# Kernel tuning notes

Hardware: AMD Instinct MI355X
Metric: run time of the kernel (lower is better)

Reference implementation:

```python
import jax, jax.numpy as jnp
import numpy as np

S, B, H, DIN = 2048, 64, 1024, 1024

def setup_inputs() -> dict:
    key = jax.random.key(0)
    ks = jax.random.split(key, 6)
    return {
        "x": jax.random.normal(ks[0], (1, B, DIN), dtype=jnp.float32),
        "last_hidden": jax.random.normal(ks[1], (1, B, H), dtype=jnp.float32),
        "encoder_outputs": jax.random.normal(ks[2], (S, B, H), dtype=jnp.float32),
        "W_ih": jax.random.normal(ks[3], (3 * H, DIN + H), dtype=jnp.float32) * 0.02,
        "W_hh": jax.random.normal(ks[4], (3 * H, H), dtype=jnp.float32) * 0.02,
        "b_ih": jnp.zeros((3 * H,), dtype=jnp.float32),
        "b_hh": jnp.zeros((3 * H,), dtype=jnp.float32),
        "batch_size": B,
    }

def reference(x, last_hidden, encoder_outputs, W_ih, W_hh, b_ih, b_hh, batch_size):
    h = last_hidden[-1]                                   # [B, H]
    # 'dot' attention: energy[b, s] = <h[b], enc[s, b]>
    scores = jnp.einsum('bh,sbh->bs', h, encoder_outputs)  # [B, S]
    attn = jax.nn.softmax(scores, axis=1)                  # [B, S]
    attn_weights = attn[:, None, :]                        # [B, 1, S]
    context = jnp.einsum('bs,sbh->bh', attn, encoder_outputs)[None]  # [1, B, H]
    rnn_input = jnp.concatenate([x, context], axis=2)[0]   # [B, DIN+H]
    # single-step PyTorch GRU cell
    gi = rnn_input @ W_ih.T + b_ih                         # [B, 3H]
    gh = h @ W_hh.T + b_hh                                 # [B, 3H]
    i_r, i_z, i_n = jnp.split(gi, 3, axis=-1)
    h_r, h_z, h_n = jnp.split(gh, 3, axis=-1)
    r = jax.nn.sigmoid(i_r + h_r)
    z = jax.nn.sigmoid(i_z + h_z)
    n = jnp.tanh(i_n + r * h_n)
    h_new = (1.0 - z) * n + z * h                          # [B, H]
    output = h_new                                         # squeeze(0)
    hidden = h_new[None]                                   # [1, B, H]
    return output, hidden, attn_weights
```

## Files before the change

### kernel.cpp

```cpp
#include <hip/hip_runtime.h>
#include <math.h>

#define S_LEN 2048
#define B_SZ  64
#define H_SZ  1024

__global__ void k_scores(const float* __restrict__ h, const float* __restrict__ enc,
                         float* __restrict__ scores) {
    int w    = blockIdx.x * 4 + (threadIdx.x >> 6);
    int lane = threadIdx.x & 63;
    int b = w >> 11;
    int s = w & 2047;
    const float* erow = enc + ((size_t)s * B_SZ + b) * H_SZ;
    const float* hrow = h + (size_t)b * H_SZ;
    float acc = 0.f;
#pragma unroll
    for (int i = 0; i < 4; ++i) {
        float4 e  = *(const float4*)(erow + i * 256 + lane * 4);
        float4 hh = *(const float4*)(hrow + i * 256 + lane * 4);
        acc += e.x * hh.x + e.y * hh.y + e.z * hh.z + e.w * hh.w;
    }
#pragma unroll
    for (int off = 32; off > 0; off >>= 1) acc += __shfl_xor(acc, off);
    if (lane == 0) scores[(size_t)b * S_LEN + s] = acc;
}

__global__ void k_softmax(const float* __restrict__ scores, float* __restrict__ attn) {
    int b = blockIdx.x, tid = threadIdx.x;
    __shared__ float sm[8];
    float v[8];
    float m = -1e30f;
#pragma unroll
    for (int i = 0; i < 8; ++i) {
        v[i] = scores[(size_t)b * S_LEN + tid + i * 256];
        m = fmaxf(m, v[i]);
    }
#pragma unroll
    for (int off = 32; off > 0; off >>= 1) m = fmaxf(m, __shfl_xor(m, off));
    if ((tid & 63) == 0) sm[tid >> 6] = m;
    __syncthreads();
    m = fmaxf(fmaxf(sm[0], sm[1]), fmaxf(sm[2], sm[3]));
    float l = 0.f;
#pragma unroll
    for (int i = 0; i < 8; ++i) { v[i] = expf(v[i] - m); l += v[i]; }
#pragma unroll
    for (int off = 32; off > 0; off >>= 1) l += __shfl_xor(l, off);
    __syncthreads();
    if ((tid & 63) == 0) sm[4 + (tid >> 6)] = l;
    __syncthreads();
    l = sm[4] + sm[5] + sm[6] + sm[7];
    float inv = 1.f / l;
#pragma unroll
    for (int i = 0; i < 8; ++i)
        attn[(size_t)b * S_LEN + tid + i * 256] = v[i] * inv;
}

__global__ void k_zero(float* __restrict__ p) {
    int idx = (blockIdx.x * 256 + threadIdx.x) * 4;
    float4 z = {0.f, 0.f, 0.f, 0.f};
    *(float4*)(p + idx) = z;
}

__global__ void k_context(const float* __restrict__ attn, const float* __restrict__ enc,
                          float* __restrict__ ctx) {
    int b = blockIdx.x;
    int chunk = blockIdx.y;
    int tid = threadIdx.x;
    float4 acc = {0.f, 0.f, 0.f, 0.f};
    int s0 = chunk * 64;
    for (int s = s0; s < s0 + 64; ++s) {
        float w  = attn[(size_t)b * S_LEN + s];
        float4 e = *(const float4*)(enc + ((size_t)s * B_SZ + b) * H_SZ + tid * 4);
        acc.x += w * e.x; acc.y += w * e.y; acc.z += w * e.z; acc.w += w * e.w;
    }
    float* dst = ctx + (size_t)b * H_SZ + tid * 4;
    atomicAdd(dst + 0, acc.x);
    atomicAdd(dst + 1, acc.y);
    atomicAdd(dst + 2, acc.z);
    atomicAdd(dst + 3, acc.w);
}

#define BK 16
#define LDP 68
__global__ __launch_bounds__(256) void k_gemm64(
    const float* __restrict__ A0, const float* __restrict__ A1,
    const float* __restrict__ W, float* __restrict__ Cpart,
    int K, int KS) {
    __shared__ float As[BK * LDP];
    __shared__ float Ws[BK * LDP];
    int jt = blockIdx.x;
    int ks = blockIdx.y;
    int tid = threadIdx.x;
    int klen = K / KS;
    int kbeg = ks * klen, kend = kbeg + klen;
    int lb = tid >> 2;
    int kq = tid & 3;
    int ty = tid >> 4;
    int tx = tid & 15;
    float acc[4][4] = {};
    for (int k0 = kbeg; k0 < kend; k0 += BK) {
        int k = k0 + kq * 4;
        const float* asrc = (k < 1024) ? (A0 + (size_t)lb * 1024 + k)
                                       : (A1 + (size_t)lb * 1024 + (k - 1024));
        float4 a = *(const float4*)asrc;
        As[(kq * 4 + 0) * LDP + lb] = a.x;
        As[(kq * 4 + 1) * LDP + lb] = a.y;
        As[(kq * 4 + 2) * LDP + lb] = a.z;
        As[(kq * 4 + 3) * LDP + lb] = a.w;
        float4 wv = *(const float4*)(W + (size_t)(jt * 64 + lb) * K + k);
        Ws[(kq * 4 + 0) * LDP + lb] = wv.x;
        Ws[(kq * 4 + 1) * LDP + lb] = wv.y;
        Ws[(kq * 4 + 2) * LDP + lb] = wv.z;
        Ws[(kq * 4 + 3) * LDP + lb] = wv.w;
        __syncthreads();
#pragma unroll
        for (int kk = 0; kk < BK; ++kk) {
            float4 a4 = *(const float4*)&As[kk * LDP + ty * 4];
            float4 w4 = *(const float4*)&Ws[kk * LDP + tx * 4];
            acc[0][0] += a4.x * w4.x; acc[0][1] += a4.x * w4.y; acc[0][2] += a4.x * w4.z; acc[0][3] += a4.x * w4.w;
            acc[1][0] += a4.y * w4.x; acc[1][1] += a4.y * w4.y; acc[1][2] += a4.y * w4.z; acc[1][3] += a4.y * w4.w;
            acc[2][0] += a4.z * w4.x; acc[2][1] += a4.z * w4.y; acc[2][2] += a4.z * w4.z; acc[2][3] += a4.z * w4.w;
            acc[3][0] += a4.w * w4.x; acc[3][1] += a4.w * w4.y; acc[3][2] += a4.w * w4.z; acc[3][3] += a4.w * w4.w;
        }
        __syncthreads();
    }
#pragma unroll
    for (int i = 0; i < 4; ++i) {
        float4 o = {acc[i][0], acc[i][1], acc[i][2], acc[i][3]};
        *(float4*)(Cpart + ((size_t)(ks * 64 + ty * 4 + i)) * 3072 + jt * 64 + tx * 4) = o;
    }
}

__global__ void k_gates(const float* __restrict__ gip, const float* __restrict__ ghp,
                        const float* __restrict__ b_ih, const float* __restrict__ b_hh,
                        const float* __restrict__ h, float* __restrict__ out) {
    int idx = blockIdx.x * 256 + threadIdx.x;
    int b = idx >> 10, j = idx & 1023;
    float ir = 0.f, iz = 0.f, in_ = 0.f, hr = 0.f, hz = 0.f, hn = 0.f;
#pragma unroll
    for (int ks = 0; ks < 4; ++ks) {
        const float* gi = gip + (size_t)(ks * 64 + b) * 3072;
        ir  += gi[j]; iz += gi[1024 + j]; in_ += gi[2048 + j];
        const float* gh = ghp + (size_t)(ks * 64 + b) * 3072;
        hr  += gh[j]; hz += gh[1024 + j]; hn += gh[2048 + j];
    }
    ir += b_ih[j]; iz += b_ih[1024 + j]; in_ += b_ih[2048 + j];
    hr += b_hh[j]; hz += b_hh[1024 + j]; hn += b_hh[2048 + j];
    float r = 1.f / (1.f + expf(-(ir + hr)));
    float z = 1.f / (1.f + expf(-(iz + hz)));
    float n = tanhf(in_ + r * hn);
    float hprev = h[idx];
    float hnew = (1.f - z) * n + z * hprev;
    out[idx] = hnew;
    out[65536 + idx] = hnew;
}

extern "C" void kernel_launch(void* const* d_in, const int* in_sizes, int n_in,
                              void* d_out, int out_size, void* d_ws, size_t ws_size,
                              hipStream_t stream) {
    const float* x    = (const float*)d_in[0];
    const float* h    = (const float*)d_in[1];
    const float* enc  = (const float*)d_in[2];
    const float* W_ih = (const float*)d_in[3];
    const float* W_hh = (const float*)d_in[4];
    const float* b_ih = (const float*)d_in[5];
    const float* b_hh = (const float*)d_in[6];
    float* out = (float*)d_out;
    float* ws  = (float*)d_ws;

    float* scores = ws;
    float* ctx    = ws + 131072;
    float* gip    = ws + 131072 + 65536;
    float* ghp    = gip + 786432;
    float* attn   = out + 131072;

    k_scores <<<32768, 256, 0, stream>>>(h, enc, scores);
    k_softmax<<<64,    256, 0, stream>>>(scores, attn);
    k_zero   <<<64,    256, 0, stream>>>(ctx);
    k_context<<<dim3(64, 32), 256, 0, stream>>>(attn, enc, ctx);
    k_gemm64 <<<dim3(48, 4),  256, 0, stream>>>(x, ctx, W_ih, gip, 2048, 4);
    k_gemm64 <<<dim3(48, 4),  256, 0, stream>>>(h, h,    W_hh, ghp, 1024, 4);
    k_gates  <<<256,   256, 0, stream>>>(gip, ghp, b_ih, b_hh, h, out);
}
```

Measured before the change: 873.1 us.

## Fuse scores, softmax and context into single-pass online-softmax attention kernel

Replaces the separate scores, softmax, zero and context kernels with one flash-style kernel. Each wave streams its encoder rows once, computing the dot-product scores and a running max/sum-rescaled context accumulator, then writes partials. A small combine kernel merges the partials and writes attn and ctx. This halves the reads of the 512MB encoder tensor and drops the atomics, at the cost of an extra partial buffer and less parallelism (1024 blocks). The GEMM k-split also goes from 4 to 8, and the gates use fast __expf.

```diff
diff --git a/kernel.cpp b/kernel.cpp
--- a/kernel.cpp
+++ b/kernel.cpp
@@ -5,93 +5,90 @@
 #define B_SZ  64
 #define H_SZ  1024
 
-__global__ void k_scores(const float* __restrict__ h, const float* __restrict__ enc,
-                         float* __restrict__ scores) {
-    int w    = blockIdx.x * 4 + (threadIdx.x >> 6);
-    int lane = threadIdx.x & 63;
-    int b = w >> 11;
-    int s = w & 2047;
-    const float* erow = enc + ((size_t)s * B_SZ + b) * H_SZ;
+__global__ __launch_bounds__(256) void k_attn(
+    const float* __restrict__ h, const float* __restrict__ enc,
+    float* __restrict__ scores, float* __restrict__ m_ws, float* __restrict__ l_ws,
+    float* __restrict__ part) {
+    int b     = blockIdx.x;
+    int chunk = blockIdx.y;
+    int widx  = threadIdx.x >> 6;
+    int lane  = threadIdx.x & 63;
     const float* hrow = h + (size_t)b * H_SZ;
-    float acc = 0.f;
+    float4 h4[4];
 #pragma unroll
-    for (int i = 0; i < 4; ++i) {
-        float4 e  = *(const float4*)(erow + i * 256 + lane * 4);
-        float4 hh = *(const float4*)(hrow + i * 256 + lane * 4);
-        acc += e.x * hh.x + e.y * hh.y + e.z * hh.z + e.w * hh.w;
+    for (int i = 0; i < 4; ++i) h4[i] = *(const float4*)(hrow + i * 256 + lane * 4);
+    float4 cacc[4] = {};
+    float m = -1e30f, l = 0.f;
+    int s0 = chunk * 128 + widx * 32;
+    for (int s = s0; s < s0 + 32; ++s) {
+        const float* erow = enc + ((size_t)s * B_SZ + b) * H_SZ;
+        float4 e[4];
+#pragma unroll
+        for (int i = 0; i < 4; ++i) e[i] = *(const float4*)(erow + i * 256 + lane * 4);
+        float d = 0.f;
+#pragma unroll
+        for (int i = 0; i < 4; ++i)
+            d += e[i].x * h4[i].x + e[i].y * h4[i].y + e[i].z * h4[i].z + e[i].w * h4[i].w;
+#pragma unroll
+        for (int off = 32; off > 0; off >>= 1) d += __shfl_xor(d, off);
+        if (lane == (s & 63)) scores[(size_t)b * S_LEN + s] = d;
+        float nm    = fmaxf(m, d);
+        float alpha = __expf(m - nm);
+        float p     = __expf(d - nm);
+        l = l * alpha + p;
+#pragma unroll
+        for (int i = 0; i < 4; ++i) {
+            cacc[i].x = cacc[i].x * alpha + p * e[i].x;
+            cacc[i].y = cacc[i].y * alpha + p * e[i].y;
+            cacc[i].z = cacc[i].z * alpha + p * e[i].z;
+            cacc[i].w = cacc[i].w * alpha + p * e[i].w;
+        }
+        m = nm;
     }
+    int wg = ((b * 16 + chunk) << 2) + widx;
+    if (lane == 0) { m_ws[wg] = m; l_ws[wg] = l; }
+    float* pd = part + (size_t)wg * H_SZ;
 #pragma unroll
-    for (int off = 32; off > 0; off >>= 1) acc += __shfl_xor(acc, off);
-    if (lane == 0) scores[(size_t)b * S_LEN + s] = acc;
+    for (int i = 0; i < 4; ++i) *(float4*)(pd + i * 256 + lane * 4) = cacc[i];
 }
 
-__global__ void k_softmax(const float* __restrict__ scores, float* __restrict__ attn) {
+__global__ void k_combine(const float* __restrict__ m_ws, const float* __restrict__ l_ws,
+                          const float* __restrict__ part, const float* __restrict__ scores,
+                          float* __restrict__ ctx, float* __restrict__ attn) {
     int b = blockIdx.x, tid = threadIdx.x;
-    __shared__ float sm[8];
-    float v[8];
-    float m = -1e30f;
+    float M = -1e30f;
+    for (int j = 0; j < 64; ++j) M = fmaxf(M, m_ws[b * 64 + j]);
+    float L = 0.f;
+    for (int j = 0; j < 64; ++j) L += l_ws[b * 64 + j] * __expf(m_ws[b * 64 + j] - M);
+    float invL = 1.f / L;
+    float4 c = {0.f, 0.f, 0.f, 0.f};
+    for (int j = 0; j < 64; ++j) {
+        float coef = __expf(m_ws[b * 64 + j] - M);
+        float4 p4 = *(const float4*)(part + ((size_t)(b * 64 + j)) * H_SZ + tid * 4);
+        c.x += coef * p4.x; c.y += coef * p4.y; c.z += coef * p4.z; c.w += coef * p4.w;
+    }
+    c.x *= invL; c.y *= invL; c.z *= invL; c.w *= invL;
+    *(float4*)(ctx + (size_t)b * H_SZ + tid * 4) = c;
 #pragma unroll
     for (int i = 0; i < 8; ++i) {
-        v[i] = scores[(size_t)b * S_LEN + tid + i * 256];
-        m = fmaxf(m, v[i]);
+        int s = tid + i * 256;
+        attn[(size_t)b * S_LEN + s] = __expf(scores[(size_t)b * S_LEN + s] - M) * invL;
     }
-#pragma unroll
-    for (int off = 32; off > 0; off >>= 1) m = fmaxf(m, __shfl_xor(m, off));
-    if ((tid & 63) == 0) sm[tid >> 6] = m;
-    __syncthreads();
-    m = fmaxf(fmaxf(sm[0], sm[1]), fmaxf(sm[2], sm[3]));
-    float l = 0.f;
-#pragma unroll
-    for (int i = 0; i < 8; ++i) { v[i] = expf(v[i] - m); l += v[i]; }
-#pragma unroll
-    for (int off = 32; off > 0; off >>= 1) l += __shfl_xor(l, off);
-    __syncthreads();
-    if ((tid & 63) == 0) sm[4 + (tid >> 6)] = l;
-    __syncthreads();
-    l = sm[4] + sm[5] + sm[6] + sm[7];
-    float inv = 1.f / l;
-#pragma unroll
-    for (int i = 0; i < 8; ++i)
-        attn[(size_t)b * S_LEN + tid + i * 256] = v[i] * inv;
-}
-
-__global__ void k_zero(float* __restrict__ p) {
-    int idx = (blockIdx.x * 256 + threadIdx.x) * 4;
-    float4 z = {0.f, 0.f, 0.f, 0.f};
-    *(float4*)(p + idx) = z;
-}
-
-__global__ void k_context(const float* __restrict__ attn, const float* __restrict__ enc,
-                          float* __restrict__ ctx) {
-    int b = blockIdx.x;
-    int chunk = blockIdx.y;
-    int tid = threadIdx.x;
-    float4 acc = {0.f, 0.f, 0.f, 0.f};
-    int s0 = chunk * 64;
-    for (int s = s0; s < s0 + 64; ++s) {
-        float w  = attn[(size_t)b * S_LEN + s];
-        float4 e = *(const float4*)(enc + ((size_t)s * B_SZ + b) * H_SZ + tid * 4);
-        acc.x += w * e.x; acc.y += w * e.y; acc.z += w * e.z; acc.w += w * e.w;
-    }
-    float* dst = ctx + (size_t)b * H_SZ + tid * 4;
-    atomicAdd(dst + 0, acc.x);
-    atomicAdd(dst + 1, acc.y);
-    atomicAdd(dst + 2, acc.z);
-    atomicAdd(dst + 3, acc.w);
 }
 
 #define BK 16
 #define LDP 68
+#define KSPLIT 8
 __global__ __launch_bounds__(256) void k_gemm64(
     const float* __restrict__ A0, const float* __restrict__ A1,
     const float* __restrict__ W, float* __restrict__ Cpart,
-    int K, int KS) {
+    int K) {
     __shared__ float As[BK * LDP];
     __shared__ float Ws[BK * LDP];
     int jt = blockIdx.x;
     int ks = blockIdx.y;
     int tid = threadIdx.x;
-    int klen = K / KS;
+    int klen = K / KSPLIT;
     int kbeg = ks * klen, kend = kbeg + klen;
     int lb = tid >> 2;
     int kq = tid & 3;
@@ -138,7 +135,7 @@
     int b = idx >> 10, j = idx & 1023;
     float ir = 0.f, iz = 0.f, in_ = 0.f, hr = 0.f, hz = 0.f, hn = 0.f;
 #pragma unroll
-    for (int ks = 0; ks < 4; ++ks) {
+    for (int ks = 0; ks < KSPLIT; ++ks) {
         const float* gi = gip + (size_t)(ks * 64 + b) * 3072;
         ir  += gi[j]; iz += gi[1024 + j]; in_ += gi[2048 + j];
         const float* gh = ghp + (size_t)(ks * 64 + b) * 3072;
@@ -146,8 +143,8 @@
     }
     ir += b_ih[j]; iz += b_ih[1024 + j]; in_ += b_ih[2048 + j];
     hr += b_hh[j]; hz += b_hh[1024 + j]; hn += b_hh[2048 + j];
-    float r = 1.f / (1.f + expf(-(ir + hr)));
-    float z = 1.f / (1.f + expf(-(iz + hz)));
+    float r = 1.f / (1.f + __expf(-(ir + hr)));
+    float z = 1.f / (1.f + __expf(-(iz + hz)));
     float n = tanhf(in_ + r * hn);
     float hprev = h[idx];
     float hnew = (1.f - z) * n + z * hprev;
@@ -169,16 +166,17 @@
     float* ws  = (float*)d_ws;
 
     float* scores = ws;
-    float* ctx    = ws + 131072;
-    float* gip    = ws + 131072 + 65536;
-    float* ghp    = gip + 786432;
+    float* ctx    = scores + 131072;
+    float* m_ws   = ctx + 65536;
+    float* l_ws   = m_ws + 4096;
+    float* part   = l_ws + 4096;
+    float* gip    = part + 4096 * 1024;
+    float* ghp    = gip + 8 * 64 * 3072;
     float* attn   = out + 131072;
 
-    k_scores <<<32768, 256, 0, stream>>>(h, enc, scores);
-    k_softmax<<<64,    256, 0, stream>>>(scores, attn);
-    k_zero   <<<64,    256, 0, stream>>>(ctx);
-    k_context<<<dim3(64, 32), 256, 0, stream>>>(attn, enc, ctx);
-    k_gemm64 <<<dim3(48, 4),  256, 0, stream>>>(x, ctx, W_ih, gip, 2048, 4);
-    k_gemm64 <<<dim3(48, 4),  256, 0, stream>>>(h, h,    W_hh, ghp, 1024, 4);
-    k_gates  <<<256,   256, 0, stream>>>(gip, ghp, b_ih, b_hh, h, out);
+    k_attn   <<<dim3(64, 16), 256, 0, stream>>>(h, enc, scores, m_ws, l_ws, part);
+    k_combine<<<64, 256, 0, stream>>>(m_ws, l_ws, part, scores, ctx, attn);
+    k_gemm64 <<<dim3(48, KSPLIT), 256, 0, stream>>>(x, ctx, W_ih, gip, 2048);
+    k_gemm64 <<<dim3(48, KSPLIT), 256, 0, stream>>>(h, h,    W_hh, ghp, 1024);
+    k_gates  <<<256, 256, 0, stream>>>(gip, ghp, b_ih, b_hh, h, out);
 }
```

Result: faster. 776.2 us (-11.1%).
